# Performance work log

Measured on AMD Instinct MI355X. Metric: run time of the kernel, lower is better.

Reference implementation:

```python
import jax, jax.numpy as jnp
import numpy as np

WIND = 5
PYR_W = (1.0, 0.5, 0.25, 0.125)
# torch bicubic (a=-0.75), scale 0.5, align_corners=False: frac offset is always 0.5
# -> fixed separable 4-tap kernel, taps at src indices 2i-1..2i+2 (edge-clamped)
BICUBIC_TAPS = (-0.09375, 0.59375, 0.59375, -0.09375)


def _windows(x):
    # x: (B,1,H,W) -> (B,25,H,W); window index k = di*5+dj, value = zero-padded x[h+di, w+dj]
    B, _, H, W = x.shape
    p = jnp.pad(x[:, 0], ((0, 0), (2, 2), (2, 2)))
    return jnp.stack([p[:, di:di + H, dj:dj + W]
                      for di in range(WIND) for dj in range(WIND)], axis=1)


def _down2_axis(a, axis):
    pad = [(0, 0)] * a.ndim
    pad[axis] = (1, 2)  # taps 2i-1..2i+2, replicate border like torch
    p = jnp.pad(a, pad, mode='edge')
    Ho = a.shape[axis] // 2
    out = None
    for k, w in enumerate(BICUBIC_TAPS):
        idx = [slice(None)] * a.ndim
        idx[axis] = slice(k, k + 2 * Ho, 2)
        t = w * p[tuple(idx)]
        out = t if out is None else out + t
    return out


def _down2(x):
    # bicubic downsample by 2 on (B,C,H,W), matching F.interpolate(scale_factor=0.5, mode='bicubic')
    return _down2_axis(_down2_axis(x, 2), 3)


def _level_loss(fake, hdr, window, rw):
    # window: (1,25,1,1) (all-ones, not normalized in the bilateral branch)
    weights_map = window * rw                                   # (B,25,H,W)
    wsum = jnp.sum(weights_map, axis=1, keepdims=True)          # (B,1,H,W)
    fake_bf = jnp.sum(_windows(fake) * weights_map, axis=1, keepdims=True) / wsum
    hdr_bf = jnp.sum(_windows(hdr) * weights_map, axis=1, keepdims=True) / wsum
    return jnp.mean((fake_bf - jax.lax.stop_gradient(hdr_bf)) ** 2)


def setup_inputs() -> dict:
    key = jax.random.key(0)
    ks = jax.random.split(key, 8)
    B, H, W = 8, 512, 512
    inp = {
        'fake': jax.random.uniform(ks[0], (B, 1, H, W), dtype=jnp.float32),
        'hdr_input': jax.random.uniform(ks[1], (B, 1, H, W), dtype=jnp.float32),
        'window': jnp.ones((1, WIND * WIND, 1, 1), dtype=jnp.float32),
    }
    for i in range(4):
        s = H >> i
        inp[f'r_weights_{i}'] = jax.random.uniform(ks[2 + i], (B, WIND * WIND, s, s), dtype=jnp.float32)
    return inp


def reference(fake, hdr_input, window, r_weights_0, r_weights_1, r_weights_2, r_weights_3):
    rws = (r_weights_0, r_weights_1, r_weights_2, r_weights_3)
    total = jnp.float32(0.0)
    f, h = fake, hdr_input
    for pw, rw in zip(PYR_W, rws):
        total = total + pw * _level_loss(f, h, window, rw)
        f = _down2(f)
        h = _down2(h)
    return total
```

## Files before the change

### kernel.cpp

```cpp
#include <hip/hip_runtime.h>
#include <hip/hip_bf16.h>

#define WT0 (-0.09375f)
#define WT1 (0.59375f)

template <int S>
__global__ __launch_bounds__(256) void loss_down_kernel(
    const float* __restrict__ F0, const float* __restrict__ H0,
    const float* __restrict__ window, const float* __restrict__ RW,
    double* __restrict__ slots, float scale,
    float* __restrict__ fd, float* __restrict__ hd)
{
    constexpr int TW = 256;
    __shared__ __align__(16) float sf[8][TW + 4];
    __shared__ __align__(16) float sh[8][TW + 4];
    __shared__ float swin[25];
    __shared__ float wred[4];

    const int tid = threadIdx.x;
    const int tx = tid & 63, ty = tid >> 6;
    if (tid < 25) swin[tid] = window[tid];

    const int bx0 = blockIdx.x * TW;
    const int by0 = blockIdx.y * 4;
    const int b   = blockIdx.z;

    const float* Fb = F0 + (size_t)b * S * S;
    const float* Hb = H0 + (size_t)b * S * S;

    for (int i = tid; i < 8 * (TW + 4); i += 256) {
        const int r = i / (TW + 4), c = i % (TW + 4);
        const int y = by0 + r - 2, x = bx0 + c - 2;
        float fv = 0.f, hv = 0.f;
        if ((unsigned)y < (unsigned)S && (unsigned)x < (unsigned)S) {
            const size_t id = (size_t)y * S + x;
            fv = Fb[id]; hv = Hb[id];
        }
        sf[r][c] = fv; sh[r][c] = hv;
    }
    __syncthreads();

    const int x0 = bx0 + 4 * tx, y = by0 + ty;
    const size_t ks = (size_t)S * S;
    const float* rwp = RW + (size_t)b * 25 * ks + (size_t)y * S + x0;

    float wsum[4] = {0.f, 0.f, 0.f, 0.f};
    float fs[4]   = {0.f, 0.f, 0.f, 0.f};
    float hs[4]   = {0.f, 0.f, 0.f, 0.f};
#pragma unroll
    for (int di = 0; di < 5; ++di) {
        float f9[9], h9[9];
        {
            const float4* pf = (const float4*)&sf[ty + di][4 * tx];
            const float4 a0 = pf[0], a1 = pf[1];
            f9[0]=a0.x; f9[1]=a0.y; f9[2]=a0.z; f9[3]=a0.w;
            f9[4]=a1.x; f9[5]=a1.y; f9[6]=a1.z; f9[7]=a1.w;
            f9[8]=sf[ty + di][4 * tx + 8];
            const float4* ph = (const float4*)&sh[ty + di][4 * tx];
            const float4 b0 = ph[0], b1 = ph[1];
            h9[0]=b0.x; h9[1]=b0.y; h9[2]=b0.z; h9[3]=b0.w;
            h9[4]=b1.x; h9[5]=b1.y; h9[6]=b1.z; h9[7]=b1.w;
            h9[8]=sh[ty + di][4 * tx + 8];
        }
#pragma unroll
        for (int dj = 0; dj < 5; ++dj) {
            const int k = di * 5 + dj;
            const float4 rv = *(const float4*)(rwp + (size_t)k * ks);
            const float w0 = swin[k] * rv.x;
            const float w1 = swin[k] * rv.y;
            const float w2 = swin[k] * rv.z;
            const float w3 = swin[k] * rv.w;
            wsum[0] += w0; wsum[1] += w1; wsum[2] += w2; wsum[3] += w3;
            fs[0] = fmaf(w0, f9[dj + 0], fs[0]);
            fs[1] = fmaf(w1, f9[dj + 1], fs[1]);
            fs[2] = fmaf(w2, f9[dj + 2], fs[2]);
            fs[3] = fmaf(w3, f9[dj + 3], fs[3]);
            hs[0] = fmaf(w0, h9[dj + 0], hs[0]);
            hs[1] = fmaf(w1, h9[dj + 1], hs[1]);
            hs[2] = fmaf(w2, h9[dj + 2], hs[2]);
            hs[3] = fmaf(w3, h9[dj + 3], hs[3]);
        }
    }
    float v = 0.f;
#pragma unroll
    for (int p = 0; p < 4; ++p) {
        const float d = (fs[p] - hs[p]) / wsum[p];
        v = fmaf(d, d, v);
    }
#pragma unroll
    for (int off = 32; off > 0; off >>= 1) v += __shfl_down(v, off, 64);
    if ((tid & 63) == 0) wred[tid >> 6] = v;

    {
        constexpr int Sh = S / 2;
        const float wt[4] = {WT0, WT1, WT1, WT0};
        for (int i = tid; i < 512; i += 256) {
            const int img = i >> 8, t2 = i & 255;
            const int r = t2 >> 7, c = t2 & 127;
            const int g1y = (by0 >> 1) + r, g1x = (bx0 >> 1) + c;
            float (*s)[TW + 4] = img ? sh : sf;
            int lc[4];
#pragma unroll
            for (int kx = 0; kx < 4; ++kx)
                lc[kx] = min(max(bx0 + 2 * c - 1 + kx, 0), S - 1) - bx0 + 2;
            float acc = 0.f;
#pragma unroll
            for (int ky = 0; ky < 4; ++ky) {
                const int lr = min(max(by0 + 2 * r - 1 + ky, 0), S - 1) - by0 + 2;
                const float rs = WT0 * (s[lr][lc[0]] + s[lr][lc[3]])
                               + WT1 * (s[lr][lc[1]] + s[lr][lc[2]]);
                acc = fmaf(wt[ky], rs, acc);
            }
            float* dst = img ? hd : fd;
            dst[((size_t)b * Sh + g1y) * Sh + g1x] = acc;
        }
    }

    __syncthreads();
    if (tid == 0) {
        const float sB = wred[0] + wred[1] + wred[2] + wred[3];
        const unsigned lin = blockIdx.x + gridDim.x * (blockIdx.y + gridDim.y * blockIdx.z);
        slots[lin] = (double)sB * (double)scale;
    }
}

__global__ __launch_bounds__(256) void loss_tail_kernel(
    const float* __restrict__ window,
    const float* __restrict__ rw2, const float* __restrict__ rw3,
    const float* __restrict__ f2, const float* __restrict__ h2,
    double* __restrict__ slots)
{
    __shared__ float s2f[8][132];
    __shared__ float s2h[8][132];
    __shared__ float p2[2][18][128];
    __shared__ float l3[2][8][68];
    __shared__ float swin[25];
    __shared__ float wred[4];

    const int tid = threadIdx.x;
    const int tx = tid & 63, ty = tid >> 6;
    if (tid < 25) swin[tid] = window[tid];
    const int lin = blockIdx.x;

    float v = 0.f;
    float scale;

    if (lin < 256) {
        const int b = lin >> 5, by0 = (lin & 31) * 4;
        const float* Fb = f2 + (size_t)b * 128 * 128;
        const float* Hb = h2 + (size_t)b * 128 * 128;
        for (int i = tid; i < 8 * 132; i += 256) {
            const int r = i / 132, c = i % 132;
            const int y = by0 + r - 2, x = c - 2;
            float fv = 0.f, hv = 0.f;
            if ((unsigned)y < 128u && (unsigned)x < 128u) {
                const size_t id = (size_t)y * 128 + x;
                fv = Fb[id]; hv = Hb[id];
            }
            s2f[r][c] = fv; s2h[r][c] = hv;
        }
        __syncthreads();

        const int x0 = 2 * tx, y = by0 + ty;
        const size_t ks = 128 * 128;
        const float* rwp = rw2 + (size_t)b * 25 * ks + (size_t)y * 128 + x0;
        float wsum[2] = {0.f, 0.f}, fs[2] = {0.f, 0.f}, hs[2] = {0.f, 0.f};
#pragma unroll
        for (int di = 0; di < 5; ++di) {
            float f6[6], h6[6];
            const float2* pf = (const float2*)&s2f[ty + di][2 * tx];
            const float2 a0 = pf[0], a1 = pf[1], a2 = pf[2];
            f6[0]=a0.x; f6[1]=a0.y; f6[2]=a1.x; f6[3]=a1.y; f6[4]=a2.x; f6[5]=a2.y;
            const float2* ph = (const float2*)&s2h[ty + di][2 * tx];
            const float2 b0 = ph[0], b1 = ph[1], b2 = ph[2];
            h6[0]=b0.x; h6[1]=b0.y; h6[2]=b1.x; h6[3]=b1.y; h6[4]=b2.x; h6[5]=b2.y;
#pragma unroll
            for (int dj = 0; dj < 5; ++dj) {
                const int k = di * 5 + dj;
                const float2 rv = *(const float2*)(rwp + (size_t)k * ks);
                const float w0 = swin[k] * rv.x;
                const float w1 = swin[k] * rv.y;
                wsum[0] += w0; wsum[1] += w1;
                fs[0] = fmaf(w0, f6[dj + 0], fs[0]);
                fs[1] = fmaf(w1, f6[dj + 1], fs[1]);
                hs[0] = fmaf(w0, h6[dj + 0], hs[0]);
                hs[1] = fmaf(w1, h6[dj + 1], hs[1]);
            }
        }
        const float d0 = (fs[0] - hs[0]) / wsum[0];
        const float d1 = (fs[1] - hs[1]) / wsum[1];
        v = fmaf(d0, d0, d1 * d1);
        scale = 0.25f / (8.f * 128.f * 128.f);
    } else {
        const int t = lin - 256;
        const int b = t >> 4, by0 = (t & 15) * 4;
        const int fr0 = 2 * by0 - 5;
        for (int i = tid; i < 2 * 18 * 128; i += 256) {
            const int img = i / 2304, j = i % 2304;
            const int r = j >> 7, c = j & 127;
            const int gy = min(max(fr0 + r, 0), 127);
            p2[img][r][c] = (img ? h2 : f2)[((size_t)b * 128 + gy) * 128 + c];
        }
        __syncthreads();
        const float wt[4] = {WT0, WT1, WT1, WT0};
        for (int i = tid; i < 2 * 8 * 68; i += 256) {
            const int img = i / 544, j = i % 544;
            const int r = j / 68, c = j % 68;
            const int gy = by0 - 2 + r, gx = c - 2;
            float a = 0.f;
            if ((unsigned)gy < 64u && (unsigned)gx < 64u) {
                int ry[4], cx[4];
#pragma unroll
                for (int k = 0; k < 4; ++k) {
                    ry[k] = min(max(2 * gy - 1 + k, 0), 127) - fr0;
                    cx[k] = min(max(2 * gx - 1 + k, 0), 127);
                }
#pragma unroll
                for (int ky = 0; ky < 4; ++ky) {
                    const float* row = p2[img][ry[ky]];
                    const float rs = WT0 * (row[cx[0]] + row[cx[3]])
                                   + WT1 * (row[cx[1]] + row[cx[2]]);
                    a = fmaf(wt[ky], rs, a);
                }
            }
            l3[img][r][c] = a;
        }
        __syncthreads();

        const size_t ks = 64 * 64;
        const float* rwp = rw3 + (size_t)b * 25 * ks + (size_t)(by0 + ty) * 64 + tx;
        float wsum = 0.f, fs = 0.f, hs = 0.f;
#pragma unroll
        for (int di = 0; di < 5; ++di) {
#pragma unroll
            for (int dj = 0; dj < 5; ++dj) {
                const int k = di * 5 + dj;
                const float wm = swin[k] * rwp[(size_t)k * ks];
                wsum += wm;
                fs = fmaf(wm, l3[0][ty + di][tx + dj], fs);
                hs = fmaf(wm, l3[1][ty + di][tx + dj], hs);
            }
        }
        const float d = (fs - hs) / wsum;
        v = d * d;
        scale = 0.125f / (8.f * 64.f * 64.f);
    }

#pragma unroll
    for (int off = 32; off > 0; off >>= 1) v += __shfl_down(v, off, 64);
    if ((tid & 63) == 0) wred[tid >> 6] = v;
    __syncthreads();
    if (tid == 0) {
        const float sB = wred[0] + wred[1] + wred[2] + wred[3];
        slots[lin] = (double)sB * (double)scale;
    }
}

__global__ void finalize_kernel(const double* __restrict__ slots, float* __restrict__ out, int n)
{
    __shared__ double dred[4];
    const int t = threadIdx.x;
    double s = 0.0;
    for (int i = t; i < n; i += 256) s += slots[i];
#pragma unroll
    for (int off = 32; off > 0; off >>= 1) s += __shfl_down(s, off, 64);
    if ((t & 63) == 0) dred[t >> 6] = s;
    __syncthreads();
    if (t == 0) out[0] = (float)(dred[0] + dred[1] + dred[2] + dred[3]);
}

extern "C" void kernel_launch(void* const* d_in, const int* in_sizes, int n_in,
                              void* d_out, int out_size, void* d_ws, size_t ws_size,
                              hipStream_t stream)
{
    const float* fake   = (const float*)d_in[0];
    const float* hdr    = (const float*)d_in[1];
    const float* window = (const float*)d_in[2];
    const float* rw0    = (const float*)d_in[3];
    const float* rw1    = (const float*)d_in[4];
    const float* rw2    = (const float*)d_in[5];
    const float* rw3    = (const float*)d_in[6];
    float* out = (float*)d_out;

    const int B = 8;
    char* ws = (char*)d_ws;
    double* slots = (double*)ws;
    float* f1 = (float*)(ws + 32768);
    const size_t n1 = (size_t)B * 256 * 256;
    float* h1 = f1 + n1;
    float* f2 = h1 + n1;
    const size_t n2 = (size_t)B * 128 * 128;
    float* h2 = f2 + n2;

    loss_down_kernel<512><<<dim3(2, 128, B), 256, 0, stream>>>(
        fake, hdr, window, rw0, slots, 1.0f / (8.f * 512.f * 512.f), f1, h1);

    loss_down_kernel<256><<<dim3(1, 64, B), 256, 0, stream>>>(
        f1, h1, window, rw1, slots + 2048, 0.5f / (8.f * 256.f * 256.f), f2, h2);

    loss_tail_kernel<<<dim3(384), 256, 0, stream>>>(
        window, rw2, rw3, f2, h2, slots + 2560);

    finalize_kernel<<<1, 256, 0, stream>>>(slots, out, 2944);
}
```

Before: 70.25 us.

## Shrink tiles for lower pyramid levels, use nontemporal weight loads, add launch bounds

After: 112.8 us. +60.6%, slower.

```diff
diff --git a/kernel.cpp b/kernel.cpp
--- a/kernel.cpp
+++ b/kernel.cpp
@@ -4,101 +4,141 @@
 #define WT0 (-0.09375f)
 #define WT1 (0.59375f)
 
-template <int S>
-__global__ __launch_bounds__(256) void loss_down_kernel(
-    const float* __restrict__ F0, const float* __restrict__ H0,
-    const float* __restrict__ window, const float* __restrict__ RW,
-    double* __restrict__ slots, float scale,
-    float* __restrict__ fd, float* __restrict__ hd)
-{
-    constexpr int TW = 256;
-    __shared__ __align__(16) float sf[8][TW + 4];
-    __shared__ __align__(16) float sh[8][TW + 4];
-    __shared__ float swin[25];
-    __shared__ float wred[4];
-
-    const int tid = threadIdx.x;
+typedef float f4v __attribute__((ext_vector_type(4)));
+typedef float f2v __attribute__((ext_vector_type(2)));
+
+template <int S, int PX>
+__device__ __forceinline__ float bilat_tile(
+    const float* __restrict__ Fb, const float* __restrict__ Hb,
+    const float* __restrict__ rwB,
+    float* __restrict__ sf, float* __restrict__ sh,
+    const float* __restrict__ swin,
+    int bx0, int by0, int tid)
+{
+    constexpr int TW = 64 * PX;
+    constexpr int LW = TW + 4;
     const int tx = tid & 63, ty = tid >> 6;
-    if (tid < 25) swin[tid] = window[tid];
-
-    const int bx0 = blockIdx.x * TW;
-    const int by0 = blockIdx.y * 4;
-    const int b   = blockIdx.z;
-
-    const float* Fb = F0 + (size_t)b * S * S;
-    const float* Hb = H0 + (size_t)b * S * S;
-
-    for (int i = tid; i < 8 * (TW + 4); i += 256) {
-        const int r = i / (TW + 4), c = i % (TW + 4);
+
+    for (int i = tid; i < 8 * LW; i += 256) {
+        const int r = i / LW, c = i % LW;
         const int y = by0 + r - 2, x = bx0 + c - 2;
         float fv = 0.f, hv = 0.f;
         if ((unsigned)y < (unsigned)S && (unsigned)x < (unsigned)S) {
             const size_t id = (size_t)y * S + x;
             fv = Fb[id]; hv = Hb[id];
         }
-        sf[r][c] = fv; sh[r][c] = hv;
+        sf[r * LW + c] = fv; sh[r * LW + c] = hv;
     }
     __syncthreads();
 
-    const int x0 = bx0 + 4 * tx, y = by0 + ty;
+    const int x0 = bx0 + PX * tx, y = by0 + ty;
     const size_t ks = (size_t)S * S;
-    const float* rwp = RW + (size_t)b * 25 * ks + (size_t)y * S + x0;
-
-    float wsum[4] = {0.f, 0.f, 0.f, 0.f};
-    float fs[4]   = {0.f, 0.f, 0.f, 0.f};
-    float hs[4]   = {0.f, 0.f, 0.f, 0.f};
+    const float* rwp = rwB + (size_t)y * S + x0;
+
+    float wsum[PX], fs[PX], hs[PX];
+#pragma unroll
+    for (int p = 0; p < PX; ++p) { wsum[p] = 0.f; fs[p] = 0.f; hs[p] = 0.f; }
+
 #pragma unroll
     for (int di = 0; di < 5; ++di) {
-        float f9[9], h9[9];
-        {
-            const float4* pf = (const float4*)&sf[ty + di][4 * tx];
-            const float4 a0 = pf[0], a1 = pf[1];
-            f9[0]=a0.x; f9[1]=a0.y; f9[2]=a0.z; f9[3]=a0.w;
-            f9[4]=a1.x; f9[5]=a1.y; f9[6]=a1.z; f9[7]=a1.w;
-            f9[8]=sf[ty + di][4 * tx + 8];
-            const float4* ph = (const float4*)&sh[ty + di][4 * tx];
-            const float4 b0 = ph[0], b1 = ph[1];
-            h9[0]=b0.x; h9[1]=b0.y; h9[2]=b0.z; h9[3]=b0.w;
-            h9[4]=b1.x; h9[5]=b1.y; h9[6]=b1.z; h9[7]=b1.w;
-            h9[8]=sh[ty + di][4 * tx + 8];
+        float f9[PX + 4], h9[PX + 4];
+        const int ro = (ty + di) * LW + PX * tx;
+        if constexpr (PX == 4) {
+            const f4v a0 = *(const f4v*)&sf[ro], a1 = *(const f4v*)&sf[ro + 4];
+            f9[0]=a0[0]; f9[1]=a0[1]; f9[2]=a0[2]; f9[3]=a0[3];
+            f9[4]=a1[0]; f9[5]=a1[1]; f9[6]=a1[2]; f9[7]=a1[3];
+            const f4v b0 = *(const f4v*)&sh[ro], b1 = *(const f4v*)&sh[ro + 4];
+            h9[0]=b0[0]; h9[1]=b0[1]; h9[2]=b0[2]; h9[3]=b0[3];
+            h9[4]=b1[0]; h9[5]=b1[1]; h9[6]=b1[2]; h9[7]=b1[3];
+        } else if constexpr (PX == 2) {
+            const f2v a0 = *(const f2v*)&sf[ro], a1 = *(const f2v*)&sf[ro + 2],
+                      a2 = *(const f2v*)&sf[ro + 4];
+            f9[0]=a0[0]; f9[1]=a0[1]; f9[2]=a1[0]; f9[3]=a1[1]; f9[4]=a2[0]; f9[5]=a2[1];
+            const f2v b0 = *(const f2v*)&sh[ro], b1 = *(const f2v*)&sh[ro + 2],
+                      b2 = *(const f2v*)&sh[ro + 4];
+            h9[0]=b0[0]; h9[1]=b0[1]; h9[2]=b1[0]; h9[3]=b1[1]; h9[4]=b2[0]; h9[5]=b2[1];
+        } else {
+#pragma unroll
+            for (int j = 0; j < 5; ++j) { f9[j] = sf[ro + j]; h9[j] = sh[ro + j]; }
         }
 #pragma unroll
         for (int dj = 0; dj < 5; ++dj) {
             const int k = di * 5 + dj;
-            const float4 rv = *(const float4*)(rwp + (size_t)k * ks);
-            const float w0 = swin[k] * rv.x;
-            const float w1 = swin[k] * rv.y;
-            const float w2 = swin[k] * rv.z;
-            const float w3 = swin[k] * rv.w;
-            wsum[0] += w0; wsum[1] += w1; wsum[2] += w2; wsum[3] += w3;
-            fs[0] = fmaf(w0, f9[dj + 0], fs[0]);
-            fs[1] = fmaf(w1, f9[dj + 1], fs[1]);
-            fs[2] = fmaf(w2, f9[dj + 2], fs[2]);
-            fs[3] = fmaf(w3, f9[dj + 3], fs[3]);
-            hs[0] = fmaf(w0, h9[dj + 0], hs[0]);
-            hs[1] = fmaf(w1, h9[dj + 1], hs[1]);
-            hs[2] = fmaf(w2, h9[dj + 2], hs[2]);
-            hs[3] = fmaf(w3, h9[dj + 3], hs[3]);
+            float rv[PX];
+            if constexpr (PX == 4) {
+                const f4v t4 = __builtin_nontemporal_load((const f4v*)(rwp + (size_t)k * ks));
+                rv[0]=t4[0]; rv[1]=t4[1]; rv[2]=t4[2]; rv[3]=t4[3];
+            } else if constexpr (PX == 2) {
+                const f2v t2 = __builtin_nontemporal_load((const f2v*)(rwp + (size_t)k * ks));
+                rv[0]=t2[0]; rv[1]=t2[1];
+            } else {
+                rv[0] = __builtin_nontemporal_load(rwp + (size_t)k * ks);
+            }
+#pragma unroll
+            for (int p = 0; p < PX; ++p) {
+                const float wm = swin[k] * rv[p];
+                wsum[p] += wm;
+                fs[p] = fmaf(wm, f9[dj + p], fs[p]);
+                hs[p] = fmaf(wm, h9[dj + p], hs[p]);
+            }
         }
     }
     float v = 0.f;
 #pragma unroll
-    for (int p = 0; p < 4; ++p) {
+    for (int p = 0; p < PX; ++p) {
         const float d = (fs[p] - hs[p]) / wsum[p];
         v = fmaf(d, d, v);
     }
+    return v;
+}
+
+__device__ __forceinline__ void reduce_and_store(
+    float v, float scale, int tid, float* wred, double* slot)
+{
 #pragma unroll
     for (int off = 32; off > 0; off >>= 1) v += __shfl_down(v, off, 64);
     if ((tid & 63) == 0) wred[tid >> 6] = v;
+    __syncthreads();
+    if (tid == 0) {
+        const float s = wred[0] + wred[1] + wred[2] + wred[3];
+        *slot = (double)s * (double)scale;
+    }
+}
+
+template <int S, int PX, int MINW>
+__global__ __launch_bounds__(256, MINW) void loss_down_kernel(
+    const float* __restrict__ F0, const float* __restrict__ H0,
+    const float* __restrict__ window, const float* __restrict__ RW,
+    double* __restrict__ slots, float scale,
+    float* __restrict__ fd, float* __restrict__ hd)
+{
+    constexpr int TW = 64 * PX, LW = TW + 4;
+    __shared__ __align__(16) float sf[8 * LW];
+    __shared__ __align__(16) float sh[8 * LW];
+    __shared__ float swin[25];
+    __shared__ float wred[4];
+
+    const int tid = threadIdx.x;
+    if (tid < 25) swin[tid] = window[tid];
+
+    constexpr int tilesX = S / TW, tilesY = S / 4, per = tilesX * tilesY;
+    const int lin = blockIdx.x;
+    const int b = lin / per, q = lin % per;
+    const int bx0 = (q % tilesX) * TW, by0 = (q / tilesX) * 4;
+
+    const float v = bilat_tile<S, PX>(
+        F0 + (size_t)b * S * S, H0 + (size_t)b * S * S,
+        RW + (size_t)b * 25 * S * S, sf, sh, swin, bx0, by0, tid);
 
     {
         constexpr int Sh = S / 2;
         const float wt[4] = {WT0, WT1, WT1, WT0};
-        for (int i = tid; i < 512; i += 256) {
-            const int img = i >> 8, t2 = i & 255;
-            const int r = t2 >> 7, c = t2 & 127;
-            const int g1y = (by0 >> 1) + r, g1x = (bx0 >> 1) + c;
-            float (*s)[TW + 4] = img ? sh : sf;
+        float* const fdb = fd + (size_t)b * Sh * Sh;
+        float* const hdb = hd + (size_t)b * Sh * Sh;
+        for (int i = tid; i < 2 * TW; i += 256) {
+            const int img = i / TW, t2 = i % TW;
+            const int r = t2 / (TW / 2), c = t2 % (TW / 2);
+            const float* s = img ? sh : sf;
             int lc[4];
 #pragma unroll
             for (int kx = 0; kx < 4; ++kx)
@@ -107,33 +147,24 @@
 #pragma unroll
             for (int ky = 0; ky < 4; ++ky) {
                 const int lr = min(max(by0 + 2 * r - 1 + ky, 0), S - 1) - by0 + 2;
-                const float rs = WT0 * (s[lr][lc[0]] + s[lr][lc[3]])
-                               + WT1 * (s[lr][lc[1]] + s[lr][lc[2]]);
+                const float rs = WT0 * (s[lr * LW + lc[0]] + s[lr * LW + lc[3]])
+                               + WT1 * (s[lr * LW + lc[1]] + s[lr * LW + lc[2]]);
                 acc = fmaf(wt[ky], rs, acc);
             }
-            float* dst = img ? hd : fd;
-            dst[((size_t)b * Sh + g1y) * Sh + g1x] = acc;
-        }
-    }
-
-    __syncthreads();
-    if (tid == 0) {
-        const float sB = wred[0] + wred[1] + wred[2] + wred[3];
-        const unsigned lin = blockIdx.x + gridDim.x * (blockIdx.y + gridDim.y * blockIdx.z);
-        slots[lin] = (double)sB * (double)scale;
-    }
-}
-
-__global__ __launch_bounds__(256) void loss_tail_kernel(
+            (img ? hdb : fdb)[((size_t)((by0 >> 1) + r)) * Sh + ((bx0 >> 1) + c)] = acc;
+        }
+    }
+
+    reduce_and_store(v, scale, tid, wred, &slots[lin]);
+}
+
+__global__ __launch_bounds__(256, 4) void loss_tail_kernel(
     const float* __restrict__ window,
     const float* __restrict__ rw2, const float* __restrict__ rw3,
     const float* __restrict__ f2, const float* __restrict__ h2,
     double* __restrict__ slots)
 {
-    __shared__ float s2f[8][132];
-    __shared__ float s2h[8][132];
-    __shared__ float p2[2][18][128];
-    __shared__ float l3[2][8][68];
+    __shared__ float smem[5696];
     __shared__ float swin[25];
     __shared__ float wred[4];
 
@@ -142,64 +173,26 @@
     if (tid < 25) swin[tid] = window[tid];
     const int lin = blockIdx.x;
 
-    float v = 0.f;
-    float scale;
-
-    if (lin < 256) {
-        const int b = lin >> 5, by0 = (lin & 31) * 4;
-        const float* Fb = f2 + (size_t)b * 128 * 128;
-        const float* Hb = h2 + (size_t)b * 128 * 128;
-        for (int i = tid; i < 8 * 132; i += 256) {
-            const int r = i / 132, c = i % 132;
-            const int y = by0 + r - 2, x = c - 2;
-            float fv = 0.f, hv = 0.f;
-            if ((unsigned)y < 128u && (unsigned)x < 128u) {
-                const size_t id = (size_t)y * 128 + x;
-                fv = Fb[id]; hv = Hb[id];
-            }
-            s2f[r][c] = fv; s2h[r][c] = hv;
-        }
-        __syncthreads();
-
-        const int x0 = 2 * tx, y = by0 + ty;
-        const size_t ks = 128 * 128;
-        const float* rwp = rw2 + (size_t)b * 25 * ks + (size_t)y * 128 + x0;
-        float wsum[2] = {0.f, 0.f}, fs[2] = {0.f, 0.f}, hs[2] = {0.f, 0.f};
-#pragma unroll
-        for (int di = 0; di < 5; ++di) {
-            float f6[6], h6[6];
-            const float2* pf = (const float2*)&s2f[ty + di][2 * tx];
-            const float2 a0 = pf[0], a1 = pf[1], a2 = pf[2];
-            f6[0]=a0.x; f6[1]=a0.y; f6[2]=a1.x; f6[3]=a1.y; f6[4]=a2.x; f6[5]=a2.y;
-            const float2* ph = (const float2*)&s2h[ty + di][2 * tx];
-            const float2 b0 = ph[0], b1 = ph[1], b2 = ph[2];
-            h6[0]=b0.x; h6[1]=b0.y; h6[2]=b1.x; h6[3]=b1.y; h6[4]=b2.x; h6[5]=b2.y;
-#pragma unroll
-            for (int dj = 0; dj < 5; ++dj) {
-                const int k = di * 5 + dj;
-                const float2 rv = *(const float2*)(rwp + (size_t)k * ks);
-                const float w0 = swin[k] * rv.x;
-                const float w1 = swin[k] * rv.y;
-                wsum[0] += w0; wsum[1] += w1;
-                fs[0] = fmaf(w0, f6[dj + 0], fs[0]);
-                fs[1] = fmaf(w1, f6[dj + 1], fs[1]);
-                hs[0] = fmaf(w0, h6[dj + 0], hs[0]);
-                hs[1] = fmaf(w1, h6[dj + 1], hs[1]);
-            }
-        }
-        const float d0 = (fs[0] - hs[0]) / wsum[0];
-        const float d1 = (fs[1] - hs[1]) / wsum[1];
-        v = fmaf(d0, d0, d1 * d1);
+    float v, scale;
+    if (lin < 512) {
+        const int b = lin >> 6, q = lin & 63;
+        const int bx0 = (q & 1) * 64, by0 = (q >> 1) * 4;
+        v = bilat_tile<128, 1>(
+            f2 + (size_t)b * 16384, h2 + (size_t)b * 16384,
+            rw2 + (size_t)b * 25 * 16384,
+            smem, smem + 544, swin, bx0, by0, tid);
         scale = 0.25f / (8.f * 128.f * 128.f);
     } else {
-        const int t = lin - 256;
+        const int t = lin - 512;
         const int b = t >> 4, by0 = (t & 15) * 4;
+        float* p2 = smem;
+        float* l3 = smem + 4608;
         const int fr0 = 2 * by0 - 5;
         for (int i = tid; i < 2 * 18 * 128; i += 256) {
             const int img = i / 2304, j = i % 2304;
             const int r = j >> 7, c = j & 127;
             const int gy = min(max(fr0 + r, 0), 127);
-            p2[img][r][c] = (img ? h2 : f2)[((size_t)b * 128 + gy) * 128 + c];
+            p2[i] = (img ? h2 : f2)[((size_t)b * 128 + gy) * 128 + c];
         }
         __syncthreads();
         const float wt[4] = {WT0, WT1, WT1, WT0};
@@ -217,43 +210,36 @@
                 }
 #pragma unroll
                 for (int ky = 0; ky < 4; ++ky) {
-                    const float* row = p2[img][ry[ky]];
+                    const float* row = p2 + img * 2304 + ry[ky] * 128;
                     const float rs = WT0 * (row[cx[0]] + row[cx[3]])
                                    + WT1 * (row[cx[1]] + row[cx[2]]);
                     a = fmaf(wt[ky], rs, a);
                 }
             }
-            l3[img][r][c] = a;
+            l3[i] = a;
         }
         __syncthreads();
 
         const size_t ks = 64 * 64;
         const float* rwp = rw3 + (size_t)b * 25 * ks + (size_t)(by0 + ty) * 64 + tx;
-        float wsum = 0.f, fs = 0.f, hs = 0.f;
+        float wsum = 0.f, fsv = 0.f, hsv = 0.f;
 #pragma unroll
         for (int di = 0; di < 5; ++di) {
 #pragma unroll
             for (int dj = 0; dj < 5; ++dj) {
                 const int k = di * 5 + dj;
-                const float wm = swin[k] * rwp[(size_t)k * ks];
+                const float wm = swin[k] * __builtin_nontemporal_load(rwp + (size_t)k * ks);
                 wsum += wm;
-                fs = fmaf(wm, l3[0][ty + di][tx + dj], fs);
-                hs = fmaf(wm, l3[1][ty + di][tx + dj], hs);
-            }
-        }
-        const float d = (fs - hs) / wsum;
+                fsv = fmaf(wm, l3[0 * 544 + (ty + di) * 68 + (tx + dj)], fsv);
+                hsv = fmaf(wm, l3[1 * 544 + (ty + di) * 68 + (tx + dj)], hsv);
+            }
+        }
+        const float d = (fsv - hsv) / wsum;
         v = d * d;
         scale = 0.125f / (8.f * 64.f * 64.f);
     }
 
-#pragma unroll
-    for (int off = 32; off > 0; off >>= 1) v += __shfl_down(v, off, 64);
-    if ((tid & 63) == 0) wred[tid >> 6] = v;
-    __syncthreads();
-    if (tid == 0) {
-        const float sB = wred[0] + wred[1] + wred[2] + wred[3];
-        slots[lin] = (double)sB * (double)scale;
-    }
+    reduce_and_store(v, scale, tid, wred, &slots[lin]);
 }
 
 __global__ void finalize_kernel(const double* __restrict__ slots, float* __restrict__ out, int n)
@@ -292,14 +278,14 @@
     const size_t n2 = (size_t)B * 128 * 128;
     float* h2 = f2 + n2;
 
-    loss_down_kernel<512><<<dim3(2, 128, B), 256, 0, stream>>>(
+    loss_down_kernel<512, 4, 1><<<dim3(2048), 256, 0, stream>>>(
         fake, hdr, window, rw0, slots, 1.0f / (8.f * 512.f * 512.f), f1, h1);
 
-    loss_down_kernel<256><<<dim3(1, 64, B), 256, 0, stream>>>(
+    loss_down_kernel<256, 2, 8><<<dim3(1024), 256, 0, stream>>>(
         f1, h1, window, rw1, slots + 2048, 0.5f / (8.f * 256.f * 256.f), f2, h2);
 
-    loss_tail_kernel<<<dim3(384), 256, 0, stream>>>(
-        window, rw2, rw3, f2, h2, slots + 2560);
-
-    finalize_kernel<<<1, 256, 0, stream>>>(slots, out, 2944);
-}
+    loss_tail_kernel<<<dim3(640), 256, 0, stream>>>(
+        window, rw2, rw3, f2, h2, slots + 3072);
+
+    finalize_kernel<<<1, 256, 0, stream>>>(slots, out, 3712);
+}
```

## Run level-2 loss alongside level-1 by recomputing downsample from f1/h1

Applied to the files above, without the earlier changes.

New measurement: 73.76 us. +5.0%, slower.

```diff
diff --git a/kernel.cpp b/kernel.cpp
--- a/kernel.cpp
+++ b/kernel.cpp
@@ -124,16 +124,14 @@
     }
 }
 
-__global__ __launch_bounds__(256) void loss_tail_kernel(
+__global__ __launch_bounds__(256) void k2_kernel(
     const float* __restrict__ window,
-    const float* __restrict__ rw2, const float* __restrict__ rw3,
-    const float* __restrict__ f2, const float* __restrict__ h2,
+    const float* __restrict__ rw1, const float* __restrict__ rw2,
+    const float* __restrict__ f1, const float* __restrict__ h1,
+    float* __restrict__ f2, float* __restrict__ h2,
     double* __restrict__ slots)
 {
-    __shared__ float s2f[8][132];
-    __shared__ float s2h[8][132];
-    __shared__ float p2[2][18][128];
-    __shared__ float l3[2][8][68];
+    __shared__ __align__(16) float smem[6056];
     __shared__ float swin[25];
     __shared__ float wred[4];
 
@@ -142,94 +140,132 @@
     if (tid < 25) swin[tid] = window[tid];
     const int lin = blockIdx.x;
 
-    float v = 0.f;
-    float scale;
-
-    if (lin < 256) {
-        const int b = lin >> 5, by0 = (lin & 31) * 4;
-        const float* Fb = f2 + (size_t)b * 128 * 128;
-        const float* Hb = h2 + (size_t)b * 128 * 128;
-        for (int i = tid; i < 8 * 132; i += 256) {
-            const int r = i / 132, c = i % 132;
+    float v, scale;
+    if (lin < 512) {
+        constexpr int S = 256, LW = 260;
+        const int b = lin >> 6, by0 = (lin & 63) * 4;
+        float* sf = smem;
+        float* sh = smem + 2080;
+        const float* Fb = f1 + (size_t)b * S * S;
+        const float* Hb = h1 + (size_t)b * S * S;
+        for (int i = tid; i < 8 * LW; i += 256) {
+            const int r = i / LW, c = i % LW;
             const int y = by0 + r - 2, x = c - 2;
             float fv = 0.f, hv = 0.f;
-            if ((unsigned)y < 128u && (unsigned)x < 128u) {
-                const size_t id = (size_t)y * 128 + x;
+            if ((unsigned)y < (unsigned)S && (unsigned)x < (unsigned)S) {
+                const size_t id = (size_t)y * S + x;
                 fv = Fb[id]; hv = Hb[id];
             }
-            s2f[r][c] = fv; s2h[r][c] = hv;
+            sf[r * LW + c] = fv; sh[r * LW + c] = hv;
         }
         __syncthreads();
 
-        const int x0 = 2 * tx, y = by0 + ty;
-        const size_t ks = 128 * 128;
-        const float* rwp = rw2 + (size_t)b * 25 * ks + (size_t)y * 128 + x0;
-        float wsum[2] = {0.f, 0.f}, fs[2] = {0.f, 0.f}, hs[2] = {0.f, 0.f};
+        const int x0 = 4 * tx, y = by0 + ty;
+        const size_t ks = (size_t)S * S;
+        const float* rwp = rw1 + (size_t)b * 25 * ks + (size_t)y * S + x0;
+        float wsum[4] = {0.f,0.f,0.f,0.f}, fsv[4] = {0.f,0.f,0.f,0.f}, hsv[4] = {0.f,0.f,0.f,0.f};
 #pragma unroll
         for (int di = 0; di < 5; ++di) {
-            float f6[6], h6[6];
-            const float2* pf = (const float2*)&s2f[ty + di][2 * tx];
-            const float2 a0 = pf[0], a1 = pf[1], a2 = pf[2];
-            f6[0]=a0.x; f6[1]=a0.y; f6[2]=a1.x; f6[3]=a1.y; f6[4]=a2.x; f6[5]=a2.y;
-            const float2* ph = (const float2*)&s2h[ty + di][2 * tx];
-            const float2 b0 = ph[0], b1 = ph[1], b2 = ph[2];
-            h6[0]=b0.x; h6[1]=b0.y; h6[2]=b1.x; h6[3]=b1.y; h6[4]=b2.x; h6[5]=b2.y;
+            float f9[9], h9[9];
+            const int ro = (ty + di) * LW + 4 * tx;
+            const float4 a0 = *(const float4*)&sf[ro], a1 = *(const float4*)&sf[ro + 4];
+            f9[0]=a0.x; f9[1]=a0.y; f9[2]=a0.z; f9[3]=a0.w;
+            f9[4]=a1.x; f9[5]=a1.y; f9[6]=a1.z; f9[7]=a1.w; f9[8]=sf[ro + 8];
+            const float4 b0 = *(const float4*)&sh[ro], b1 = *(const float4*)&sh[ro + 4];
+            h9[0]=b0.x; h9[1]=b0.y; h9[2]=b0.z; h9[3]=b0.w;
+            h9[4]=b1.x; h9[5]=b1.y; h9[6]=b1.z; h9[7]=b1.w; h9[8]=sh[ro + 8];
 #pragma unroll
             for (int dj = 0; dj < 5; ++dj) {
                 const int k = di * 5 + dj;
-                const float2 rv = *(const float2*)(rwp + (size_t)k * ks);
-                const float w0 = swin[k] * rv.x;
-                const float w1 = swin[k] * rv.y;
-                wsum[0] += w0; wsum[1] += w1;
-                fs[0] = fmaf(w0, f6[dj + 0], fs[0]);
-                fs[1] = fmaf(w1, f6[dj + 1], fs[1]);
-                hs[0] = fmaf(w0, h6[dj + 0], hs[0]);
-                hs[1] = fmaf(w1, h6[dj + 1], hs[1]);
-            }
-        }
-        const float d0 = (fs[0] - hs[0]) / wsum[0];
-        const float d1 = (fs[1] - hs[1]) / wsum[1];
-        v = fmaf(d0, d0, d1 * d1);
-        scale = 0.25f / (8.f * 128.f * 128.f);
+                const float4 rv = *(const float4*)(rwp + (size_t)k * ks);
+                const float w0 = swin[k] * rv.x, w1 = swin[k] * rv.y;
+                const float w2 = swin[k] * rv.z, w3 = swin[k] * rv.w;
+                wsum[0] += w0; wsum[1] += w1; wsum[2] += w2; wsum[3] += w3;
+                fsv[0] = fmaf(w0, f9[dj + 0], fsv[0]);
+                fsv[1] = fmaf(w1, f9[dj + 1], fsv[1]);
+                fsv[2] = fmaf(w2, f9[dj + 2], fsv[2]);
+                fsv[3] = fmaf(w3, f9[dj + 3], fsv[3]);
+                hsv[0] = fmaf(w0, h9[dj + 0], hsv[0]);
+                hsv[1] = fmaf(w1, h9[dj + 1], hsv[1]);
+                hsv[2] = fmaf(w2, h9[dj + 2], hsv[2]);
+                hsv[3] = fmaf(w3, h9[dj + 3], hsv[3]);
+            }
+        }
+        v = 0.f;
+#pragma unroll
+        for (int p = 0; p < 4; ++p) {
+            const float d = (fsv[p] - hsv[p]) / wsum[p];
+            v = fmaf(d, d, v);
+        }
+        scale = 0.5f / (8.f * 256.f * 256.f);
+
+        {
+            const float wt[4] = {WT0, WT1, WT1, WT0};
+            for (int i = tid; i < 512; i += 256) {
+                const int img = i >> 8, t2 = i & 255;
+                const int r = t2 >> 7, c = t2 & 127;
+                const float* s = img ? sh : sf;
+                int lc[4];
+#pragma unroll
+                for (int kx = 0; kx < 4; ++kx)
+                    lc[kx] = min(max(2 * c - 1 + kx, 0), S - 1) + 2;
+                float acc = 0.f;
+#pragma unroll
+                for (int ky = 0; ky < 4; ++ky) {
+                    const int lr = min(max(by0 + 2 * r - 1 + ky, 0), S - 1) - by0 + 2;
+                    const float rs = WT0 * (s[lr * LW + lc[0]] + s[lr * LW + lc[3]])
+                                   + WT1 * (s[lr * LW + lc[1]] + s[lr * LW + lc[2]]);
+                    acc = fmaf(wt[ky], rs, acc);
+                }
+                float* dst = img ? h2 : f2;
+                dst[((size_t)b * 128 + ((by0 >> 1) + r)) * 128 + c] = acc;
+            }
+        }
     } else {
-        const int t = lin - 256;
-        const int b = t >> 4, by0 = (t & 15) * 4;
-        const int fr0 = 2 * by0 - 5;
-        for (int i = tid; i < 2 * 18 * 128; i += 256) {
-            const int img = i / 2304, j = i % 2304;
-            const int r = j >> 7, c = j & 127;
-            const int gy = min(max(fr0 + r, 0), 127);
-            p2[img][r][c] = (img ? h2 : f2)[((size_t)b * 128 + gy) * 128 + c];
+        const int t = lin - 512;
+        const int b = t >> 6, q = t & 63;
+        const int bx0 = (q & 1) * 64, by0 = (q >> 1) * 4;
+        float* p1 = smem;
+        float* l2 = smem + 4968;
+        const int fr0 = 2 * by0 - 5, fc0 = 2 * bx0 - 5;
+        const float* F1 = f1 + (size_t)b * 256 * 256;
+        const float* H1 = h1 + (size_t)b * 256 * 256;
+        for (int i = tid; i < 2 * 18 * 138; i += 256) {
+            const int img = i / 2484, j = i % 2484;
+            const int r = j / 138, c = j % 138;
+            const int gy = min(max(fr0 + r, 0), 255);
+            const int gx = min(max(fc0 + c, 0), 255);
+            p1[i] = (img ? H1 : F1)[(size_t)gy * 256 + gx];
         }
         __syncthreads();
         const float wt[4] = {WT0, WT1, WT1, WT0};
         for (int i = tid; i < 2 * 8 * 68; i += 256) {
             const int img = i / 544, j = i % 544;
             const int r = j / 68, c = j % 68;
-            const int gy = by0 - 2 + r, gx = c - 2;
+            const int gy = by0 - 2 + r, gx = bx0 - 2 + c;
             float a = 0.f;
-            if ((unsigned)gy < 64u && (unsigned)gx < 64u) {
+            if ((unsigned)gy < 128u && (unsigned)gx < 128u) {
                 int ry[4], cx[4];
 #pragma unroll
                 for (int k = 0; k < 4; ++k) {
-                    ry[k] = min(max(2 * gy - 1 + k, 0), 127) - fr0;
-                    cx[k] = min(max(2 * gx - 1 + k, 0), 127);
+                    ry[k] = min(max(2 * gy - 1 + k, 0), 255) - fr0;
+                    cx[k] = min(max(2 * gx - 1 + k, 0), 255) - fc0;
                 }
 #pragma unroll
                 for (int ky = 0; ky < 4; ++ky) {
-                    const float* row = p2[img][ry[ky]];
+                    const float* row = p1 + img * 2484 + ry[ky] * 138;
                     const float rs = WT0 * (row[cx[0]] + row[cx[3]])
                                    + WT1 * (row[cx[1]] + row[cx[2]]);
                     a = fmaf(wt[ky], rs, a);
                 }
             }
-            l3[img][r][c] = a;
+            l2[i] = a;
         }
         __syncthreads();
 
-        const size_t ks = 64 * 64;
-        const float* rwp = rw3 + (size_t)b * 25 * ks + (size_t)(by0 + ty) * 64 + tx;
-        float wsum = 0.f, fs = 0.f, hs = 0.f;
+        const size_t ks = 128 * 128;
+        const float* rwp = rw2 + (size_t)b * 25 * ks + (size_t)(by0 + ty) * 128 + (bx0 + tx);
+        float wsum = 0.f, fsv = 0.f, hsv = 0.f;
 #pragma unroll
         for (int di = 0; di < 5; ++di) {
 #pragma unroll
@@ -237,13 +273,13 @@
                 const int k = di * 5 + dj;
                 const float wm = swin[k] * rwp[(size_t)k * ks];
                 wsum += wm;
-                fs = fmaf(wm, l3[0][ty + di][tx + dj], fs);
-                hs = fmaf(wm, l3[1][ty + di][tx + dj], hs);
-            }
-        }
-        const float d = (fs - hs) / wsum;
+                fsv = fmaf(wm, l2[0 * 544 + (ty + di) * 68 + (tx + dj)], fsv);
+                hsv = fmaf(wm, l2[1 * 544 + (ty + di) * 68 + (tx + dj)], hsv);
+            }
+        }
+        const float d = (fsv - hsv) / wsum;
         v = d * d;
-        scale = 0.125f / (8.f * 64.f * 64.f);
+        scale = 0.25f / (8.f * 128.f * 128.f);
     }
 
 #pragma unroll
@@ -253,6 +289,82 @@
     if (tid == 0) {
         const float sB = wred[0] + wred[1] + wred[2] + wred[3];
         slots[lin] = (double)sB * (double)scale;
+    }
+}
+
+__global__ __launch_bounds__(256) void l3_kernel(
+    const float* __restrict__ window, const float* __restrict__ rw3,
+    const float* __restrict__ f2, const float* __restrict__ h2,
+    double* __restrict__ slots)
+{
+    __shared__ float p2[2 * 18 * 128];
+    __shared__ float l3[2 * 8 * 68];
+    __shared__ float swin[25];
+    __shared__ float wred[4];
+
+    const int tid = threadIdx.x;
+    const int tx = tid & 63, ty = tid >> 6;
+    if (tid < 25) swin[tid] = window[tid];
+
+    const int t = blockIdx.x;
+    const int b = t >> 4, by0 = (t & 15) * 4;
+    const int fr0 = 2 * by0 - 5;
+    for (int i = tid; i < 2 * 18 * 128; i += 256) {
+        const int img = i / 2304, j = i % 2304;
+        const int r = j >> 7, c = j & 127;
+        const int gy = min(max(fr0 + r, 0), 127);
+        p2[i] = (img ? h2 : f2)[((size_t)b * 128 + gy) * 128 + c];
+    }
+    __syncthreads();
+    const float wt[4] = {WT0, WT1, WT1, WT0};
+    for (int i = tid; i < 2 * 8 * 68; i += 256) {
+        const int img = i / 544, j = i % 544;
+        const int r = j / 68, c = j % 68;
+        const int gy = by0 - 2 + r, gx = c - 2;
+        float a = 0.f;
+        if ((unsigned)gy < 64u && (unsigned)gx < 64u) {
+            int ry[4], cx[4];
+#pragma unroll
+            for (int k = 0; k < 4; ++k) {
+                ry[k] = min(max(2 * gy - 1 + k, 0), 127) - fr0;
+                cx[k] = min(max(2 * gx - 1 + k, 0), 127);
+            }
+#pragma unroll
+            for (int ky = 0; ky < 4; ++ky) {
+                const float* row = p2 + img * 2304 + ry[ky] * 128;
+                const float rs = WT0 * (row[cx[0]] + row[cx[3]])
+                               + WT1 * (row[cx[1]] + row[cx[2]]);
+                a = fmaf(wt[ky], rs, a);
+            }
+        }
+        l3[i] = a;
+    }
+    __syncthreads();
+
+    const size_t ks = 64 * 64;
+    const float* rwp = rw3 + (size_t)b * 25 * ks + (size_t)(by0 + ty) * 64 + tx;
+    float wsum = 0.f, fsv = 0.f, hsv = 0.f;
+#pragma unroll
+    for (int di = 0; di < 5; ++di) {
+#pragma unroll
+        for (int dj = 0; dj < 5; ++dj) {
+            const int k = di * 5 + dj;
+            const float wm = swin[k] * rwp[(size_t)k * ks];
+            wsum += wm;
+            fsv = fmaf(wm, l3[0 * 544 + (ty + di) * 68 + (tx + dj)], fsv);
+            hsv = fmaf(wm, l3[1 * 544 + (ty + di) * 68 + (tx + dj)], hsv);
+        }
+    }
+    const float d = (fsv - hsv) / wsum;
+    float v = d * d;
+
+#pragma unroll
+    for (int off = 32; off > 0; off >>= 1) v += __shfl_down(v, off, 64);
+    if ((tid & 63) == 0) wred[tid >> 6] = v;
+    __syncthreads();
+    if (tid == 0) {
+        const float sB = wred[0] + wred[1] + wred[2] + wred[3];
+        slots[blockIdx.x] = (double)sB * (double)(0.125f / (8.f * 64.f * 64.f));
     }
 }
 
@@ -295,11 +407,11 @@
     loss_down_kernel<512><<<dim3(2, 128, B), 256, 0, stream>>>(
         fake, hdr, window, rw0, slots, 1.0f / (8.f * 512.f * 512.f), f1, h1);
 
-    loss_down_kernel<256><<<dim3(1, 64, B), 256, 0, stream>>>(
-        f1, h1, window, rw1, slots + 2048, 0.5f / (8.f * 256.f * 256.f), f2, h2);
-
-    loss_tail_kernel<<<dim3(384), 256, 0, stream>>>(
-        window, rw2, rw3, f2, h2, slots + 2560);
-
-    finalize_kernel<<<1, 256, 0, stream>>>(slots, out, 2944);
+    k2_kernel<<<dim3(1024), 256, 0, stream>>>(
+        window, rw1, rw2, f1, h1, f2, h2, slots + 2048);
+
+    l3_kernel<<<dim3(128), 256, 0, stream>>>(
+        window, rw3, f2, h2, slots + 3072);
+
+    finalize_kernel<<<1, 256, 0, stream>>>(slots, out, 3200);
 }
```

## Fuse level-0 and level-1 loss kernels, recomputing level-1 tiles from full-resolution input

Applied to the files above, without the earlier changes.

Result: slower. 81.54 us (+16.1%).

```diff
diff --git a/kernel.cpp b/kernel.cpp
--- a/kernel.cpp
+++ b/kernel.cpp
@@ -4,122 +4,167 @@
 #define WT0 (-0.09375f)
 #define WT1 (0.59375f)
 
-template <int S>
-__global__ __launch_bounds__(256) void loss_down_kernel(
-    const float* __restrict__ F0, const float* __restrict__ H0,
-    const float* __restrict__ window, const float* __restrict__ RW,
-    double* __restrict__ slots, float scale,
-    float* __restrict__ fd, float* __restrict__ hd)
+__global__ __launch_bounds__(256) void k1_kernel(
+    const float* __restrict__ fake, const float* __restrict__ hdr,
+    const float* __restrict__ window,
+    const float* __restrict__ rw0, const float* __restrict__ rw1,
+    float* __restrict__ f2, float* __restrict__ h2,
+    double* __restrict__ slots)
 {
-    constexpr int TW = 256;
-    __shared__ __align__(16) float sf[8][TW + 4];
-    __shared__ __align__(16) float sh[8][TW + 4];
+    __shared__ __align__(16) float smem[4160];
     __shared__ float swin[25];
     __shared__ float wred[4];
 
     const int tid = threadIdx.x;
     const int tx = tid & 63, ty = tid >> 6;
     if (tid < 25) swin[tid] = window[tid];
-
-    const int bx0 = blockIdx.x * TW;
-    const int by0 = blockIdx.y * 4;
-    const int b   = blockIdx.z;
-
-    const float* Fb = F0 + (size_t)b * S * S;
-    const float* Hb = H0 + (size_t)b * S * S;
-
-    for (int i = tid; i < 8 * (TW + 4); i += 256) {
-        const int r = i / (TW + 4), c = i % (TW + 4);
-        const int y = by0 + r - 2, x = bx0 + c - 2;
-        float fv = 0.f, hv = 0.f;
-        if ((unsigned)y < (unsigned)S && (unsigned)x < (unsigned)S) {
-            const size_t id = (size_t)y * S + x;
-            fv = Fb[id]; hv = Hb[id];
-        }
-        sf[r][c] = fv; sh[r][c] = hv;
+    const int lin = blockIdx.x;
+    const float wt[4] = {WT0, WT1, WT1, WT0};
+
+    float v, scale;
+
+    if (lin < 2048) {
+        constexpr int S = 512, LW = 260;
+        const int b = lin >> 8, t = lin & 255;
+        const int by0 = (t >> 1) * 4, bx0 = (t & 1) * 256;
+        float* sf = smem;
+        float* sh = smem + 2080;
+        const float* Fb = fake + (size_t)b * S * S;
+        const float* Hb = hdr  + (size_t)b * S * S;
+        for (int i = tid; i < 8 * LW; i += 256) {
+            const int r = i / LW, c = i % LW;
+            const int y = by0 + r - 2, x = bx0 + c - 2;
+            float fv = 0.f, hv = 0.f;
+            if ((unsigned)y < (unsigned)S && (unsigned)x < (unsigned)S) {
+                const size_t id = (size_t)y * S + x;
+                fv = Fb[id]; hv = Hb[id];
+            }
+            sf[r * LW + c] = fv; sh[r * LW + c] = hv;
+        }
+        __syncthreads();
+
+        const int x0 = bx0 + 4 * tx, y = by0 + ty;
+        const size_t ks = (size_t)S * S;
+        const float* rwp = rw0 + (size_t)b * 25 * ks + (size_t)y * S + x0;
+        float wsum[4] = {0.f,0.f,0.f,0.f}, fs[4] = {0.f,0.f,0.f,0.f}, hs[4] = {0.f,0.f,0.f,0.f};
+#pragma unroll
+        for (int di = 0; di < 5; ++di) {
+            float f9[9], h9[9];
+            const int ro = (ty + di) * LW + 4 * tx;
+            const float4 a0 = *(const float4*)&sf[ro], a1 = *(const float4*)&sf[ro + 4];
+            f9[0]=a0.x; f9[1]=a0.y; f9[2]=a0.z; f9[3]=a0.w;
+            f9[4]=a1.x; f9[5]=a1.y; f9[6]=a1.z; f9[7]=a1.w; f9[8]=sf[ro + 8];
+            const float4 b0 = *(const float4*)&sh[ro], b1 = *(const float4*)&sh[ro + 4];
+            h9[0]=b0.x; h9[1]=b0.y; h9[2]=b0.z; h9[3]=b0.w;
+            h9[4]=b1.x; h9[5]=b1.y; h9[6]=b1.z; h9[7]=b1.w; h9[8]=sh[ro + 8];
+#pragma unroll
+            for (int dj = 0; dj < 5; ++dj) {
+                const int k = di * 5 + dj;
+                const float4 rv = *(const float4*)(rwp + (size_t)k * ks);
+                const float w0 = swin[k] * rv.x, w1 = swin[k] * rv.y;
+                const float w2 = swin[k] * rv.z, w3 = swin[k] * rv.w;
+                wsum[0] += w0; wsum[1] += w1; wsum[2] += w2; wsum[3] += w3;
+                fs[0] = fmaf(w0, f9[dj + 0], fs[0]);
+                fs[1] = fmaf(w1, f9[dj + 1], fs[1]);
+                fs[2] = fmaf(w2, f9[dj + 2], fs[2]);
+                fs[3] = fmaf(w3, f9[dj + 3], fs[3]);
+                hs[0] = fmaf(w0, h9[dj + 0], hs[0]);
+                hs[1] = fmaf(w1, h9[dj + 1], hs[1]);
+                hs[2] = fmaf(w2, h9[dj + 2], hs[2]);
+                hs[3] = fmaf(w3, h9[dj + 3], hs[3]);
+            }
+        }
+        v = 0.f;
+#pragma unroll
+        for (int p = 0; p < 4; ++p) {
+            const float d = (fs[p] - hs[p]) / wsum[p];
+            v = fmaf(d, d, v);
+        }
+        scale = 1.0f / (8.f * 512.f * 512.f);
+    } else {
+        const int p = lin - 2048;
+        const int b = p >> 8, q = p & 255;
+        const int bx0 = (q & 3) * 64, by0 = (q >> 2) * 4;
+        float* sbuf = smem;
+        float* l1F  = smem + 2484;
+        float* l1H  = smem + 3028;
+        const int fr0 = 2 * by0 - 5, fc0 = 2 * bx0 - 5;
+
+        for (int img = 0; img < 2; ++img) {
+            const float* src = (img ? hdr : fake) + (size_t)b * 512 * 512;
+            float* dst = img ? l1H : l1F;
+            __syncthreads();
+            for (int i = tid; i < 18 * 138; i += 256) {
+                const int r = i / 138, c = i % 138;
+                const int gy = min(max(fr0 + r, 0), 511);
+                const int gx = min(max(fc0 + c, 0), 511);
+                sbuf[i] = src[(size_t)gy * 512 + gx];
+            }
+            __syncthreads();
+            for (int i = tid; i < 8 * 68; i += 256) {
+                const int r = i / 68, c = i % 68;
+                const int gy1 = by0 - 2 + r, gx1 = bx0 - 2 + c;
+                float a = 0.f;
+                if ((unsigned)gy1 < 256u && (unsigned)gx1 < 256u) {
+#pragma unroll
+                    for (int ky = 0; ky < 4; ++ky) {
+                        const float* row = sbuf + (2 * r + ky) * 138 + 2 * c;
+                        const float rs = WT0 * (row[0] + row[3]) + WT1 * (row[1] + row[2]);
+                        a = fmaf(wt[ky], rs, a);
+                    }
+                }
+                dst[i] = a;
+            }
+        }
+        __syncthreads();
+
+        if (tid < 128) {
+            const int img = tid >> 6, j = tid & 63;
+            const int r = j >> 5, c = j & 31;
+            const int gy2 = (by0 >> 1) + r, gx2 = (bx0 >> 1) + c;
+            const float* l1 = img ? l1H : l1F;
+            int rL[4], cL[4];
+#pragma unroll
+            for (int k = 0; k < 4; ++k) {
+                rL[k] = min(max(2 * gy2 - 1 + k, 0), 255) - (by0 - 2);
+                cL[k] = min(max(2 * gx2 - 1 + k, 0), 255) - (bx0 - 2);
+            }
+            float a = 0.f;
+#pragma unroll
+            for (int ky = 0; ky < 4; ++ky) {
+                const float* row = l1 + rL[ky] * 68;
+                const float rs = WT0 * (row[cL[0]] + row[cL[3]])
+                               + WT1 * (row[cL[1]] + row[cL[2]]);
+                a = fmaf(wt[ky], rs, a);
+            }
+            (img ? h2 : f2)[((size_t)b * 128 + gy2) * 128 + gx2] = a;
+        }
+
+        const size_t ks = 256 * 256;
+        const float* rwp = rw1 + (size_t)b * 25 * ks + (size_t)(by0 + ty) * 256 + (bx0 + tx);
+        float wsum = 0.f, fsv = 0.f, hsv = 0.f;
+#pragma unroll
+        for (int di = 0; di < 5; ++di) {
+#pragma unroll
+            for (int dj = 0; dj < 5; ++dj) {
+                const int k = di * 5 + dj;
+                const float wm = swin[k] * rwp[(size_t)k * ks];
+                wsum += wm;
+                fsv = fmaf(wm, l1F[(ty + di) * 68 + (tx + dj)], fsv);
+                hsv = fmaf(wm, l1H[(ty + di) * 68 + (tx + dj)], hsv);
+            }
+        }
+        const float d = (fsv - hsv) / wsum;
+        v = d * d;
+        scale = 0.5f / (8.f * 256.f * 256.f);
     }
-    __syncthreads();
-
-    const int x0 = bx0 + 4 * tx, y = by0 + ty;
-    const size_t ks = (size_t)S * S;
-    const float* rwp = RW + (size_t)b * 25 * ks + (size_t)y * S + x0;
-
-    float wsum[4] = {0.f, 0.f, 0.f, 0.f};
-    float fs[4]   = {0.f, 0.f, 0.f, 0.f};
-    float hs[4]   = {0.f, 0.f, 0.f, 0.f};
-#pragma unroll
-    for (int di = 0; di < 5; ++di) {
-        float f9[9], h9[9];
-        {
-            const float4* pf = (const float4*)&sf[ty + di][4 * tx];
-            const float4 a0 = pf[0], a1 = pf[1];
-            f9[0]=a0.x; f9[1]=a0.y; f9[2]=a0.z; f9[3]=a0.w;
-            f9[4]=a1.x; f9[5]=a1.y; f9[6]=a1.z; f9[7]=a1.w;
-            f9[8]=sf[ty + di][4 * tx + 8];
-            const float4* ph = (const float4*)&sh[ty + di][4 * tx];
-            const float4 b0 = ph[0], b1 = ph[1];
-            h9[0]=b0.x; h9[1]=b0.y; h9[2]=b0.z; h9[3]=b0.w;
-            h9[4]=b1.x; h9[5]=b1.y; h9[6]=b1.z; h9[7]=b1.w;
-            h9[8]=sh[ty + di][4 * tx + 8];
-        }
-#pragma unroll
-        for (int dj = 0; dj < 5; ++dj) {
-            const int k = di * 5 + dj;
-            const float4 rv = *(const float4*)(rwp + (size_t)k * ks);
-            const float w0 = swin[k] * rv.x;
-            const float w1 = swin[k] * rv.y;
-            const float w2 = swin[k] * rv.z;
-            const float w3 = swin[k] * rv.w;
-            wsum[0] += w0; wsum[1] += w1; wsum[2] += w2; wsum[3] += w3;
-            fs[0] = fmaf(w0, f9[dj + 0], fs[0]);
-            fs[1] = fmaf(w1, f9[dj + 1], fs[1]);
-            fs[2] = fmaf(w2, f9[dj + 2], fs[2]);
-            fs[3] = fmaf(w3, f9[dj + 3], fs[3]);
-            hs[0] = fmaf(w0, h9[dj + 0], hs[0]);
-            hs[1] = fmaf(w1, h9[dj + 1], hs[1]);
-            hs[2] = fmaf(w2, h9[dj + 2], hs[2]);
-            hs[3] = fmaf(w3, h9[dj + 3], hs[3]);
-        }
-    }
-    float v = 0.f;
-#pragma unroll
-    for (int p = 0; p < 4; ++p) {
-        const float d = (fs[p] - hs[p]) / wsum[p];
-        v = fmaf(d, d, v);
-    }
+
 #pragma unroll
     for (int off = 32; off > 0; off >>= 1) v += __shfl_down(v, off, 64);
     if ((tid & 63) == 0) wred[tid >> 6] = v;
-
-    {
-        constexpr int Sh = S / 2;
-        const float wt[4] = {WT0, WT1, WT1, WT0};
-        for (int i = tid; i < 512; i += 256) {
-            const int img = i >> 8, t2 = i & 255;
-            const int r = t2 >> 7, c = t2 & 127;
-            const int g1y = (by0 >> 1) + r, g1x = (bx0 >> 1) + c;
-            float (*s)[TW + 4] = img ? sh : sf;
-            int lc[4];
-#pragma unroll
-            for (int kx = 0; kx < 4; ++kx)
-                lc[kx] = min(max(bx0 + 2 * c - 1 + kx, 0), S - 1) - bx0 + 2;
-            float acc = 0.f;
-#pragma unroll
-            for (int ky = 0; ky < 4; ++ky) {
-                const int lr = min(max(by0 + 2 * r - 1 + ky, 0), S - 1) - by0 + 2;
-                const float rs = WT0 * (s[lr][lc[0]] + s[lr][lc[3]])
-                               + WT1 * (s[lr][lc[1]] + s[lr][lc[2]]);
-                acc = fmaf(wt[ky], rs, acc);
-            }
-            float* dst = img ? hd : fd;
-            dst[((size_t)b * Sh + g1y) * Sh + g1x] = acc;
-        }
-    }
-
     __syncthreads();
     if (tid == 0) {
         const float sB = wred[0] + wred[1] + wred[2] + wred[3];
-        const unsigned lin = blockIdx.x + gridDim.x * (blockIdx.y + gridDim.y * blockIdx.z);
         slots[lin] = (double)sB * (double)scale;
     }
 }
@@ -229,7 +274,7 @@
 
         const size_t ks = 64 * 64;
         const float* rwp = rw3 + (size_t)b * 25 * ks + (size_t)(by0 + ty) * 64 + tx;
-        float wsum = 0.f, fs = 0.f, hs = 0.f;
+        float wsum = 0.f, fsv = 0.f, hsv = 0.f;
 #pragma unroll
         for (int di = 0; di < 5; ++di) {
 #pragma unroll
@@ -237,11 +282,11 @@
                 const int k = di * 5 + dj;
                 const float wm = swin[k] * rwp[(size_t)k * ks];
                 wsum += wm;
-                fs = fmaf(wm, l3[0][ty + di][tx + dj], fs);
-                hs = fmaf(wm, l3[1][ty + di][tx + dj], hs);
-            }
-        }
-        const float d = (fs - hs) / wsum;
+                fsv = fmaf(wm, l3[0][ty + di][tx + dj], fsv);
+                hsv = fmaf(wm, l3[1][ty + di][tx + dj], hsv);
+            }
+        }
+        const float d = (fsv - hsv) / wsum;
         v = d * d;
         scale = 0.125f / (8.f * 64.f * 64.f);
     }
@@ -285,21 +330,15 @@
     const int B = 8;
     char* ws = (char*)d_ws;
     double* slots = (double*)ws;
-    float* f1 = (float*)(ws + 32768);
-    const size_t n1 = (size_t)B * 256 * 256;
-    float* h1 = f1 + n1;
-    float* f2 = h1 + n1;
+    float* f2 = (float*)(ws + 65536);
     const size_t n2 = (size_t)B * 128 * 128;
     float* h2 = f2 + n2;
 
-    loss_down_kernel<512><<<dim3(2, 128, B), 256, 0, stream>>>(
-        fake, hdr, window, rw0, slots, 1.0f / (8.f * 512.f * 512.f), f1, h1);
-
-    loss_down_kernel<256><<<dim3(1, 64, B), 256, 0, stream>>>(
-        f1, h1, window, rw1, slots + 2048, 0.5f / (8.f * 256.f * 256.f), f2, h2);
+    k1_kernel<<<dim3(4096), 256, 0, stream>>>(
+        fake, hdr, window, rw0, rw1, f2, h2, slots);
 
     loss_tail_kernel<<<dim3(384), 256, 0, stream>>>(
-        window, rw2, rw3, f2, h2, slots + 2560);
-
-    finalize_kernel<<<1, 256, 0, stream>>>(slots, out, 2944);
+        window, rw2, rw3, f2, h2, slots + 4096);
+
+    finalize_kernel<<<1, 256, 0, stream>>>(slots, out, 4480);
 }
```
